# Performance work log

Measured on AMD Instinct MI355X. Metric: run time of the kernel, lower is better.

Reference implementation:

```python
import jax, jax.numpy as jnp
import numpy as np

NUM_HEADS = 16
HEAD_DIM = 64
INNER = NUM_HEADS * HEAD_DIM  # 1024
QUERY_DIM = 1024
CONTEXT_DIM = 768
SCALE = HEAD_DIM ** -0.5


def setup_inputs() -> dict:
    key = jax.random.key(0)
    ks = jax.random.split(key, 6)
    B, NQ, NKV = 8, 1024, 2048
    query = jax.random.normal(ks[0], (B, NQ, QUERY_DIM), dtype=jnp.float32)
    context = jax.random.normal(ks[1], (B, NKV, CONTEXT_DIM), dtype=jnp.float32)
    # weights stored as [in, out] (transpose of torch Linear), math-equivalent
    w_q = jax.random.normal(ks[2], (QUERY_DIM, INNER), dtype=jnp.float32) * (QUERY_DIM ** -0.5)
    w_kv = jax.random.normal(ks[3], (CONTEXT_DIM, 2 * INNER), dtype=jnp.float32) * (CONTEXT_DIM ** -0.5)
    w_out = jax.random.normal(ks[4], (INNER, QUERY_DIM), dtype=jnp.float32) * (INNER ** -0.5)
    b_out = jax.random.normal(ks[5], (QUERY_DIM,), dtype=jnp.float32) * 0.01
    return {"query": query, "context": context, "w_q": w_q, "w_kv": w_kv,
            "w_out": w_out, "b_out": b_out}


def reference(query, context, w_q, w_kv, w_out, b_out):
    B, NQ, _ = query.shape
    NKV = context.shape[1]
    q = query @ w_q                              # [B, NQ, INNER]
    kv = context @ w_kv                          # [B, NKV, 2*INNER]
    k, v = jnp.split(kv, 2, axis=-1)
    # reshape to [B, H, N, D]
    q = q.reshape(B, NQ, NUM_HEADS, HEAD_DIM).transpose(0, 2, 1, 3)
    k = k.reshape(B, NKV, NUM_HEADS, HEAD_DIM).transpose(0, 2, 1, 3)
    v = v.reshape(B, NKV, NUM_HEADS, HEAD_DIM).transpose(0, 2, 1, 3)
    scores = jnp.einsum('bhqd,bhkd->bhqk', q, k) * SCALE
    attn = jax.nn.softmax(scores, axis=-1)
    out = jnp.einsum('bhqk,bhkd->bhqd', attn, v)  # [B, H, NQ, D]
    out = out.transpose(0, 2, 1, 3).reshape(B, NQ, INNER)
    return out @ w_out + b_out
```

## Files before the change

kernel.cpp:

```cpp
#include <hip/hip_runtime.h>
#include <stdint.h>

typedef __bf16 bf16_t;
typedef bf16_t bf16x8 __attribute__((ext_vector_type(8)));
typedef float f32x4 __attribute__((ext_vector_type(4)));
typedef float f32x16 __attribute__((ext_vector_type(16)));
typedef unsigned uint32x2_t __attribute__((ext_vector_type(2)));
typedef unsigned uint32x4_t __attribute__((ext_vector_type(4)));

__device__ __forceinline__ unsigned short f2bf(float x) {
    unsigned u = __builtin_bit_cast(unsigned, x);
    u = (u + 0x7FFFu + ((u >> 16) & 1u)) >> 16;
    return (unsigned short)u;
}

__device__ __forceinline__ unsigned pk_bf16(float lo, float hi) {
    unsigned u0 = __builtin_bit_cast(unsigned, lo) + 0x8000u;
    unsigned u1 = __builtin_bit_cast(unsigned, hi) + 0x8000u;
    return __builtin_amdgcn_perm(u1, u0, 0x07060302u);
}

__device__ __forceinline__ void async_load16(const void* g, void* lds) {
    auto* gp = reinterpret_cast<const __attribute__((address_space(1))) uint32_t*>(
        reinterpret_cast<uintptr_t>(g));
    auto* lp = reinterpret_cast<__attribute__((address_space(3))) uint32_t*>(
        reinterpret_cast<uintptr_t>(lds));
    __builtin_amdgcn_global_load_lds(gp, lp, 16, 0, 0);
}

__global__ __launch_bounds__(256) void cast_f32_bf16(const float* __restrict__ src,
                                                     unsigned short* __restrict__ dst,
                                                     int n8) {
    int i = blockIdx.x * 256 + threadIdx.x;
    if (i >= n8) return;
    const float4* s4 = (const float4*)src;
    float4 a = s4[i * 2], b = s4[i * 2 + 1];
    uint4 o;
    o.x = (unsigned)f2bf(a.x) | ((unsigned)f2bf(a.y) << 16);
    o.y = (unsigned)f2bf(a.z) | ((unsigned)f2bf(a.w) << 16);
    o.z = (unsigned)f2bf(b.x) | ((unsigned)f2bf(b.y) << 16);
    o.w = (unsigned)f2bf(b.z) | ((unsigned)f2bf(b.w) << 16);
    ((uint4*)dst)[i] = o;
}

__global__ __launch_bounds__(256) void transcast(const float* __restrict__ src,
                                                 unsigned short* __restrict__ dst,
                                                 int K, int N, float scale) {
    __shared__ float tile[32][33];
    int x = threadIdx.x, y = threadIdx.y;
    int c0 = blockIdx.x * 32, r0 = blockIdx.y * 32;
    #pragma unroll
    for (int i = 0; i < 32; i += 8)
        tile[y + i][x] = src[(size_t)(r0 + y + i) * N + c0 + x];
    __syncthreads();
    #pragma unroll
    for (int i = 0; i < 32; i += 8)
        dst[(size_t)(c0 + y + i) * K + r0 + x] = f2bf(tile[x][y + i] * scale);
}

template <int EPI>
__global__ __launch_bounds__(256) void gemm_bt(const unsigned short* __restrict__ A,
                                               const unsigned short* __restrict__ Bt,
                                               void* __restrict__ Cout,
                                               const float* __restrict__ bias,
                                               int K, int N, int nkt) {
    __shared__ __align__(16) unsigned short lA[2][128 * 64];
    __shared__ __align__(16) unsigned short lB[2][128 * 64];
    const int tid = threadIdx.x;
    const int w = tid >> 6, l = tid & 63;
    const int wm = w >> 1, wn = w & 1;
    const int row0 = blockIdx.y * 128, col0 = blockIdx.x * 128;
    const int lrow = l & 15, lq = l >> 4;
    const int srow = l >> 3;
    const int scol = ((l & 7) ^ srow) * 8;

    f32x4 acc[4][4];
    #pragma unroll
    for (int i = 0; i < 4; ++i)
        #pragma unroll
        for (int j = 0; j < 4; ++j) acc[i][j] = (f32x4)0.f;

    const unsigned short* ga[4];
    const unsigned short* gb[4];
    #pragma unroll
    for (int q = 0; q < 4; ++q) {
        const int r = (w * 4 + q) * 8 + srow;
        ga[q] = A + (size_t)(row0 + r) * K + scol;
        gb[q] = Bt + (size_t)(col0 + r) * K + scol;
    }

    #pragma unroll
    for (int q = 0; q < 4; ++q) {
        async_load16(ga[q], (char*)lA + (w * 4 + q) * 1024);
        async_load16(gb[q], (char*)lB + (w * 4 + q) * 1024);
        ga[q] += 64;
        gb[q] += 64;
    }
    __syncthreads();

    for (int kt = 0; kt < nkt; ++kt) {
        const int bo = (kt & 1) * 16384;
        if (kt + 1 < nkt) {
            const int bn = bo ^ 16384;
            #pragma unroll
            for (int q = 0; q < 4; ++q) {
                async_load16(ga[q], (char*)lA + bn + (w * 4 + q) * 1024);
                async_load16(gb[q], (char*)lB + bn + (w * 4 + q) * 1024);
                ga[q] += 64;
                gb[q] += 64;
            }
        }
        #pragma unroll
        for (int kc = 0; kc < 2; ++kc) {
            const int pc = ((kc * 4 + lq) ^ (lrow & 7)) * 16;
            bf16x8 af[4], bfr[4];
            #pragma unroll
            for (int i = 0; i < 4; ++i)
                af[i] = *(const bf16x8*)((const char*)lA + bo + (wm * 64 + i * 16 + lrow) * 128 + pc);
            #pragma unroll
            for (int j = 0; j < 4; ++j)
                bfr[j] = *(const bf16x8*)((const char*)lB + bo + (wn * 64 + j * 16 + lrow) * 128 + pc);
            #pragma unroll
            for (int i = 0; i < 4; ++i)
                #pragma unroll
                for (int j = 0; j < 4; ++j)
                    acc[i][j] = __builtin_amdgcn_mfma_f32_16x16x32_bf16(af[i], bfr[j],
                                                                        acc[i][j], 0, 0, 0);
        }
        __syncthreads();
    }
    #pragma unroll
    for (int i = 0; i < 4; ++i) {
        const int grow0 = row0 + wm * 64 + i * 16 + lq * 4;
        #pragma unroll
        for (int j = 0; j < 4; ++j) {
            const int gcol = col0 + wn * 64 + j * 16 + lrow;
            #pragma unroll
            for (int r = 0; r < 4; ++r) {
                float v = acc[i][j][r];
                int grow = grow0 + r;
                if (EPI == 0) {
                    ((unsigned short*)Cout)[(size_t)grow * N + gcol] = f2bf(v);
                } else {
                    ((float*)Cout)[(size_t)grow * N + gcol] = v + bias[gcol];
                }
            }
        }
    }
}

__global__ __launch_bounds__(256, 2) void gemm_kv(const unsigned short* __restrict__ A,
                                                  const unsigned short* __restrict__ Bt,
                                                  unsigned short* __restrict__ Kb,
                                                  unsigned short* __restrict__ Vt) {
    __shared__ __align__(16) unsigned short lA[256 * 64];
    __shared__ __align__(16) unsigned short lB[128 * 64];
    const int tid = threadIdx.x;
    const int w = tid >> 6, l = tid & 63;
    const int wm = w >> 1, wn = w & 1;
    const int row0 = blockIdx.y * 256, col0 = blockIdx.x * 128;
    const int r32 = l & 31, hw = l >> 5;
    const int srow = l >> 3, scol = ((l & 7) ^ srow) * 8;

    f32x16 acc[4][2];
    #pragma unroll
    for (int mi = 0; mi < 4; ++mi)
        #pragma unroll
        for (int ni = 0; ni < 2; ++ni) acc[mi][ni] = (f32x16)0.f;

    const unsigned short* ga = A + (size_t)(row0 + w * 8 + srow) * 768 + scol;
    const unsigned short* gb = Bt + (size_t)(col0 + w * 8 + srow) * 768 + scol;
    char* lAw = (char*)lA + (w * 8) * 128;
    char* lBw = (char*)lB + (w * 8) * 128;
    const char* lap = (const char*)lA + (wm * 128 + r32) * 128;
    const char* lbp = (const char*)lB + (wn * 64 + r32) * 128;
    const int r7 = r32 & 7;

    for (int kt = 0; kt < 12; ++kt) {
        __syncthreads();
        #pragma unroll
        for (int q = 0; q < 8; ++q)
            async_load16(ga + (size_t)q * 32 * 768, lAw + q * 32 * 128);
        #pragma unroll
        for (int q = 0; q < 4; ++q)
            async_load16(gb + (size_t)q * 32 * 768, lBw + q * 32 * 128);
        ga += 64;
        gb += 64;
        __syncthreads();
        #pragma unroll
        for (int ks = 0; ks < 4; ++ks) {
            const int off = ((ks * 2 + hw) ^ r7) * 16;
            bf16x8 af[4], bfr[2];
            #pragma unroll
            for (int mi = 0; mi < 4; ++mi)
                af[mi] = *(const bf16x8*)(lap + mi * 32 * 128 + off);
            #pragma unroll
            for (int ni = 0; ni < 2; ++ni)
                bfr[ni] = *(const bf16x8*)(lbp + ni * 32 * 128 + off);
            #pragma unroll
            for (int mi = 0; mi < 4; ++mi)
                #pragma unroll
                for (int ni = 0; ni < 2; ++ni)
                    acc[mi][ni] = __builtin_amdgcn_mfma_f32_32x32x16_bf16(af[mi], bfr[ni],
                                                                          acc[mi][ni], 0, 0, 0);
        }
    }

    if (col0 < 1024) {
        unsigned short* kp = Kb + (size_t)(row0 + wm * 128) * 1024 + col0 + wn * 64 + r32;
        #pragma unroll
        for (int mi = 0; mi < 4; ++mi)
            #pragma unroll
            for (int ni = 0; ni < 2; ++ni)
                #pragma unroll
                for (int reg = 0; reg < 16; ++reg) {
                    int rr = mi * 32 + (reg & 3) + 8 * (reg >> 2) + 4 * hw;
                    kp[(size_t)rr * 1024 + ni * 32] = f2bf(acc[mi][ni][reg]);
                }
    } else {
        const int bb = row0 >> 11;
        const int keybase = (row0 & 2047) + wm * 128 + 4 * hw;
        const int fvbase = col0 - 1024 + wn * 64 + r32;
        unsigned short* vp = Vt + ((size_t)bb * 1024 + fvbase) * 2048 + keybase;
        #pragma unroll
        for (int mi = 0; mi < 4; ++mi)
            #pragma unroll
            for (int ni = 0; ni < 2; ++ni)
                #pragma unroll
                for (int g = 0; g < 4; ++g) {
                    uint2 pk2;
                    pk2.x = pk_bf16(acc[mi][ni][g * 4 + 0], acc[mi][ni][g * 4 + 1]);
                    pk2.y = pk_bf16(acc[mi][ni][g * 4 + 2], acc[mi][ni][g * 4 + 3]);
                    *(uint2*)(vp + (size_t)(ni * 32) * 2048 + mi * 32 + g * 8) = pk2;
                }
    }
}

__global__ __launch_bounds__(256, 4) void attn_fwd(const unsigned short* __restrict__ qb,
                                                   const unsigned short* __restrict__ kb,
                                                   const unsigned short* __restrict__ vt,
                                                   unsigned short* __restrict__ ob) {
    __shared__ __align__(16) unsigned short lK[2][64 * 64];
    __shared__ __align__(16) unsigned short lV[2][64 * 64];
    const int tid = threadIdx.x;
    const int w = tid >> 6, l = tid & 63;
    const int bh = blockIdx.x;
    const int b = bh >> 4, h = bh & 15;
    const int q0 = blockIdx.y * 128;
    const int lrow = l & 15, lq = l >> 4;
    const int srow = l >> 3, scol = ((l & 7) ^ (srow & 7)) * 8;

    bf16x8 bq[2][2];
    #pragma unroll
    for (int u = 0; u < 2; ++u)
        #pragma unroll
        for (int kc = 0; kc < 2; ++kc) {
            int row = b * 1024 + q0 + w * 32 + u * 16 + lrow;
            int col = h * 64 + kc * 32 + lq * 8;
            bq[u][kc] = *(const bf16x8*)(qb + (size_t)row * 1024 + col);
        }

    f32x4 ot[2][4];
    f32x4 lfr[2];
    #pragma unroll
    for (int u = 0; u < 2; ++u) {
        #pragma unroll
        for (int dt = 0; dt < 4; ++dt) ot[u][dt] = (f32x4)0.f;
        lfr[u] = (f32x4)0.f;
    }
    bf16x8 one8;
    #pragma unroll
    for (int i = 0; i < 8; ++i) one8[i] = (bf16_t)1.0f;

    const char* kp0 = (const char*)lK + lrow * 128 + ((lq ^ (lrow & 7)) * 16);
    const char* kp1 = (const char*)lK + lrow * 128 + (((4 + lq) ^ (lrow & 7)) * 16);
    const char* vp0 = (const char*)lV + lrow * 128 + ((lq ^ (lrow & 7)) * 16);
    const char* vp1 = (const char*)lV + lrow * 128 + (((4 + lq) ^ (lrow & 7)) * 16);

    const unsigned short* gkp = kb + (size_t)b * 2048 * 1024 + h * 64 +
                                (size_t)(w * 8 + srow) * 1024 + scol;
    const unsigned short* gvp = vt + (size_t)(b * 1024 + h * 64) * 2048 +
                                (size_t)(w * 8 + srow) * 2048 + scol;
    char* lKw0 = (char*)lK + (w * 8) * 128;
    char* lKw1 = (char*)lK + (32 + w * 8) * 128;
    char* lVw0 = (char*)lV + (w * 8) * 128;
    char* lVw1 = (char*)lV + (32 + w * 8) * 128;

    async_load16(gkp, lKw0);
    async_load16(gkp + 32 * 1024, lKw1);
    async_load16(gvp, lVw0);
    async_load16(gvp + 32 * 2048, lVw1);
    gkp += 64 * 1024;
    gvp += 64;
    __syncthreads();

    for (int it = 0; it < 32; ++it) {
        const int bo = (it & 1) * 8192;
        if (it < 31) {
            const int bn = bo ^ 8192;
            async_load16(gkp, lKw0 + bn);
            async_load16(gkp + 32 * 1024, lKw1 + bn);
            async_load16(gvp, lVw0 + bn);
            async_load16(gvp + 32 * 2048, lVw1 + bn);
            gkp += 64 * 1024;
            gvp += 64;
        }

        bf16x8 ka[4][2];
        #pragma unroll
        for (int mt = 0; mt < 4; ++mt) {
            ka[mt][0] = *(const bf16x8*)(kp0 + bo + mt * 2048);
            ka[mt][1] = *(const bf16x8*)(kp1 + bo + mt * 2048);
        }

        unsigned D[2][4][2];
        __builtin_amdgcn_s_setprio(1);
        #pragma unroll
        for (int u = 0; u < 2; ++u) {
            #pragma unroll
            for (int mt = 0; mt < 4; ++mt) {
                f32x4 c = (f32x4)0.f;
                c = __builtin_amdgcn_mfma_f32_16x16x32_bf16(ka[mt][0], bq[u][0], c, 0, 0, 0);
                c = __builtin_amdgcn_mfma_f32_16x16x32_bf16(ka[mt][1], bq[u][1], c, 0, 0, 0);
                #pragma unroll
                for (int r = 0; r < 4; ++r)
                    c[r] = __builtin_amdgcn_exp2f(c[r]);
                D[u][mt][0] = pk_bf16(c[0], c[1]);
                D[u][mt][1] = pk_bf16(c[2], c[3]);
            }
        }
        __builtin_amdgcn_s_setprio(0);

        bf16x8 pb[2][2];
        #pragma unroll
        for (int u = 0; u < 2; ++u) {
            uint32x4_t pbw[2];
            #pragma unroll
            for (int half = 0; half < 2; ++half) {
                #pragma unroll
                for (int r2 = 0; r2 < 2; ++r2) {
                    uint32x2_t t = __builtin_amdgcn_permlane32_swap(
                        D[u][half * 2][r2], D[u][half * 2 + 1][r2], false, false);
                    uint32x2_t z = __builtin_amdgcn_permlane16_swap(t.x, t.y, false, false);
                    pbw[half][r2] = z.x;
                    pbw[half][r2 + 2] = z.y;
                }
            }
            pb[u][0] = __builtin_bit_cast(bf16x8, pbw[0]);
            pb[u][1] = __builtin_bit_cast(bf16x8, pbw[1]);
        }

        bf16x8 va[4][2];
        #pragma unroll
        for (int dt = 0; dt < 4; ++dt) {
            va[dt][0] = *(const bf16x8*)(vp0 + bo + dt * 2048);
            va[dt][1] = *(const bf16x8*)(vp1 + bo + dt * 2048);
        }

        __builtin_amdgcn_s_setprio(1);
        #pragma unroll
        for (int u = 0; u < 2; ++u) {
            lfr[u] = __builtin_amdgcn_mfma_f32_16x16x32_bf16(one8, pb[u][0], lfr[u], 0, 0, 0);
            lfr[u] = __builtin_amdgcn_mfma_f32_16x16x32_bf16(one8, pb[u][1], lfr[u], 0, 0, 0);
            #pragma unroll
            for (int dt = 0; dt < 4; ++dt) {
                ot[u][dt] = __builtin_amdgcn_mfma_f32_16x16x32_bf16(va[dt][0], pb[u][0], ot[u][dt], 0, 0, 0);
                ot[u][dt] = __builtin_amdgcn_mfma_f32_16x16x32_bf16(va[dt][1], pb[u][1], ot[u][dt], 0, 0, 0);
            }
        }
        __builtin_amdgcn_s_setprio(0);
        __syncthreads();
    }

    #pragma unroll
    for (int u = 0; u < 2; ++u) {
        float inv = 1.f / lfr[u][0];
        size_t grow = (size_t)(b * 1024 + q0 + w * 32 + u * 16 + lrow);
        unsigned short* op = ob + grow * 1024 + h * 64 + 4 * lq;
        #pragma unroll
        for (int dt = 0; dt < 4; ++dt) {
            uint2 pk;
            pk.x = pk_bf16(ot[u][dt][0] * inv, ot[u][dt][1] * inv);
            pk.y = pk_bf16(ot[u][dt][2] * inv, ot[u][dt][3] * inv);
            *(uint2*)(op + 16 * dt) = pk;
        }
    }
}

extern "C" void kernel_launch(void* const* d_in, const int* in_sizes, int n_in,
                              void* d_out, int out_size, void* d_ws, size_t ws_size,
                              hipStream_t stream) {
    const float* query   = (const float*)d_in[0];
    const float* context = (const float*)d_in[1];
    const float* w_q     = (const float*)d_in[2];
    const float* w_kv    = (const float*)d_in[3];
    const float* w_out   = (const float*)d_in[4];
    const float* b_out   = (const float*)d_in[5];
    float* out = (float*)d_out;

    char* p = (char*)d_ws;
    unsigned short* qin   = (unsigned short*)p; p += (size_t)8192 * 1024 * 2;
    unsigned short* cin   = (unsigned short*)p; p += (size_t)16384 * 768 * 2;
    unsigned short* wqT   = (unsigned short*)p; p += (size_t)1024 * 1024 * 2;
    unsigned short* wkvT  = (unsigned short*)p; p += (size_t)2048 * 768 * 2;
    unsigned short* woutT = (unsigned short*)p; p += (size_t)1024 * 1024 * 2;
    unsigned short* qproj = (unsigned short*)p; p += (size_t)8192 * 1024 * 2;
    unsigned short* kbuf  = (unsigned short*)p; p += (size_t)16384 * 1024 * 2;
    unsigned short* vT    = (unsigned short*)p; p += (size_t)16384 * 1024 * 2;
    unsigned short* obuf  = (unsigned short*)p; p += (size_t)8192 * 1024 * 2;

    const float qscale = 0.125f * 1.44269504088896f;

    cast_f32_bf16<<<8388608 / 8 / 256, 256, 0, stream>>>(query, qin, 8388608 / 8);
    cast_f32_bf16<<<12582912 / 8 / 256, 256, 0, stream>>>(context, cin, 12582912 / 8);
    transcast<<<dim3(32, 32), dim3(32, 8), 0, stream>>>(w_q, wqT, 1024, 1024, qscale);
    transcast<<<dim3(64, 24), dim3(32, 8), 0, stream>>>(w_kv, wkvT, 768, 2048, 1.0f);
    transcast<<<dim3(32, 32), dim3(32, 8), 0, stream>>>(w_out, woutT, 1024, 1024, 1.0f);
    gemm_bt<0><<<dim3(8, 64), 256, 0, stream>>>(qin, wqT, qproj, nullptr, 1024, 1024, 16);
    gemm_kv<<<dim3(16, 64), 256, 0, stream>>>(cin, wkvT, kbuf, vT);
    attn_fwd<<<dim3(128, 8), 256, 0, stream>>>(qproj, kbuf, vT, obuf);
    gemm_bt<2><<<dim3(8, 64), 256, 0, stream>>>(obuf, woutT, out, b_out, 1024, 1024, 16);
}
```

Baseline: 332.4 us.

## Fuse prep kernels, double-buffer smaller KV GEMM tiles, halve attention query tile

Merges the two casts and three weight transposes into one launch that dispatches on block index, which cuts launch overhead. The KV projection GEMM moves from 256x128 single-buffered tiles to 128x128 double-buffered tiles, prefetching the next K slice during MFMA work and doubling the grid. Attention blocks now cover 64 query rows instead of 128, with each wave holding one 16-row fragment. This doubles the grid and raises the occupancy target to 5, at the cost of loading each K/V tile twice as often per query row.

```diff
diff --git a/kernel.cpp b/kernel.cpp
--- a/kernel.cpp
+++ b/kernel.cpp
@@ -28,11 +28,8 @@
     __builtin_amdgcn_global_load_lds(gp, lp, 16, 0, 0);
 }
 
-__global__ __launch_bounds__(256) void cast_f32_bf16(const float* __restrict__ src,
-                                                     unsigned short* __restrict__ dst,
-                                                     int n8) {
-    int i = blockIdx.x * 256 + threadIdx.x;
-    if (i >= n8) return;
+__device__ __forceinline__ void cast8(const float* __restrict__ src,
+                                      unsigned short* __restrict__ dst, int i) {
     const float4* s4 = (const float4*)src;
     float4 a = s4[i * 2], b = s4[i * 2 + 1];
     uint4 o;
@@ -43,12 +40,12 @@
     ((uint4*)dst)[i] = o;
 }
 
-__global__ __launch_bounds__(256) void transcast(const float* __restrict__ src,
-                                                 unsigned short* __restrict__ dst,
-                                                 int K, int N, float scale) {
-    __shared__ float tile[32][33];
-    int x = threadIdx.x, y = threadIdx.y;
-    int c0 = blockIdx.x * 32, r0 = blockIdx.y * 32;
+__device__ __forceinline__ void transcast_body(const float* __restrict__ src,
+                                               unsigned short* __restrict__ dst,
+                                               int K, int N, float scale,
+                                               int bx, int by, float (*tile)[33],
+                                               int x, int y) {
+    int c0 = bx * 32, r0 = by * 32;
     #pragma unroll
     for (int i = 0; i < 32; i += 8)
         tile[y + i][x] = src[(size_t)(r0 + y + i) * N + c0 + x];
@@ -56,6 +53,36 @@
     #pragma unroll
     for (int i = 0; i < 32; i += 8)
         dst[(size_t)(c0 + y + i) * K + r0 + x] = f2bf(tile[x][y + i] * scale);
+}
+
+__global__ __launch_bounds__(256) void prep(const float* __restrict__ query,
+                                            const float* __restrict__ context,
+                                            const float* __restrict__ w_q,
+                                            const float* __restrict__ w_kv,
+                                            const float* __restrict__ w_out,
+                                            unsigned short* __restrict__ qin,
+                                            unsigned short* __restrict__ cin,
+                                            unsigned short* __restrict__ wqT,
+                                            unsigned short* __restrict__ wkvT,
+                                            unsigned short* __restrict__ woutT,
+                                            float qscale) {
+    __shared__ float tile[32][33];
+    const int blk = blockIdx.x, tid = threadIdx.x;
+    const int x = tid & 31, y = tid >> 5;
+    if (blk < 4096) {
+        cast8(query, qin, blk * 256 + tid);
+    } else if (blk < 10240) {
+        cast8(context, cin, (blk - 4096) * 256 + tid);
+    } else if (blk < 11264) {
+        int lb = blk - 10240;
+        transcast_body(w_q, wqT, 1024, 1024, qscale, lb & 31, lb >> 5, tile, x, y);
+    } else if (blk < 12800) {
+        int lb = blk - 11264;
+        transcast_body(w_kv, wkvT, 768, 2048, 1.0f, lb & 63, lb >> 6, tile, x, y);
+    } else {
+        int lb = blk - 12800;
+        transcast_body(w_out, woutT, 1024, 1024, 1.0f, lb & 31, lb >> 5, tile, x, y);
+    }
 }
 
 template <int EPI>
@@ -153,63 +180,72 @@
                                                   const unsigned short* __restrict__ Bt,
                                                   unsigned short* __restrict__ Kb,
                                                   unsigned short* __restrict__ Vt) {
-    __shared__ __align__(16) unsigned short lA[256 * 64];
-    __shared__ __align__(16) unsigned short lB[128 * 64];
+    __shared__ __align__(16) unsigned short lA[2][128 * 64];
+    __shared__ __align__(16) unsigned short lB[2][128 * 64];
     const int tid = threadIdx.x;
     const int w = tid >> 6, l = tid & 63;
     const int wm = w >> 1, wn = w & 1;
-    const int row0 = blockIdx.y * 256, col0 = blockIdx.x * 128;
+    const int row0 = blockIdx.y * 128, col0 = blockIdx.x * 128;
     const int r32 = l & 31, hw = l >> 5;
     const int srow = l >> 3, scol = ((l & 7) ^ srow) * 8;
-
-    f32x16 acc[4][2];
-    #pragma unroll
-    for (int mi = 0; mi < 4; ++mi)
+    const int r7 = r32 & 7;
+
+    f32x16 acc[2][2];
+    #pragma unroll
+    for (int mi = 0; mi < 2; ++mi)
         #pragma unroll
         for (int ni = 0; ni < 2; ++ni) acc[mi][ni] = (f32x16)0.f;
 
     const unsigned short* ga = A + (size_t)(row0 + w * 8 + srow) * 768 + scol;
     const unsigned short* gb = Bt + (size_t)(col0 + w * 8 + srow) * 768 + scol;
-    char* lAw = (char*)lA + (w * 8) * 128;
-    char* lBw = (char*)lB + (w * 8) * 128;
-    const char* lap = (const char*)lA + (wm * 128 + r32) * 128;
+    const char* lap = (const char*)lA + (wm * 64 + r32) * 128;
     const char* lbp = (const char*)lB + (wn * 64 + r32) * 128;
-    const int r7 = r32 & 7;
+
+    #pragma unroll
+    for (int q = 0; q < 4; ++q) {
+        async_load16(ga + (size_t)q * 32 * 768, (char*)lA + (q * 32 + w * 8) * 128);
+        async_load16(gb + (size_t)q * 32 * 768, (char*)lB + (q * 32 + w * 8) * 128);
+    }
+    ga += 64;
+    gb += 64;
+    __syncthreads();
 
     for (int kt = 0; kt < 12; ++kt) {
-        __syncthreads();
-        #pragma unroll
-        for (int q = 0; q < 8; ++q)
-            async_load16(ga + (size_t)q * 32 * 768, lAw + q * 32 * 128);
-        #pragma unroll
-        for (int q = 0; q < 4; ++q)
-            async_load16(gb + (size_t)q * 32 * 768, lBw + q * 32 * 128);
-        ga += 64;
-        gb += 64;
-        __syncthreads();
+        const int bo = (kt & 1) * 16384;
+        if (kt < 11) {
+            const int bn = bo ^ 16384;
+            #pragma unroll
+            for (int q = 0; q < 4; ++q) {
+                async_load16(ga + (size_t)q * 32 * 768, (char*)lA + bn + (q * 32 + w * 8) * 128);
+                async_load16(gb + (size_t)q * 32 * 768, (char*)lB + bn + (q * 32 + w * 8) * 128);
+            }
+            ga += 64;
+            gb += 64;
+        }
         #pragma unroll
         for (int ks = 0; ks < 4; ++ks) {
             const int off = ((ks * 2 + hw) ^ r7) * 16;
-            bf16x8 af[4], bfr[2];
-            #pragma unroll
-            for (int mi = 0; mi < 4; ++mi)
-                af[mi] = *(const bf16x8*)(lap + mi * 32 * 128 + off);
+            bf16x8 af[2], bfr[2];
+            #pragma unroll
+            for (int mi = 0; mi < 2; ++mi)
+                af[mi] = *(const bf16x8*)(lap + bo + mi * 32 * 128 + off);
             #pragma unroll
             for (int ni = 0; ni < 2; ++ni)
-                bfr[ni] = *(const bf16x8*)(lbp + ni * 32 * 128 + off);
-            #pragma unroll
-            for (int mi = 0; mi < 4; ++mi)
+                bfr[ni] = *(const bf16x8*)(lbp + bo + ni * 32 * 128 + off);
+            #pragma unroll
+            for (int mi = 0; mi < 2; ++mi)
                 #pragma unroll
                 for (int ni = 0; ni < 2; ++ni)
                     acc[mi][ni] = __builtin_amdgcn_mfma_f32_32x32x16_bf16(af[mi], bfr[ni],
                                                                           acc[mi][ni], 0, 0, 0);
         }
+        __syncthreads();
     }
 
     if (col0 < 1024) {
-        unsigned short* kp = Kb + (size_t)(row0 + wm * 128) * 1024 + col0 + wn * 64 + r32;
-        #pragma unroll
-        for (int mi = 0; mi < 4; ++mi)
+        unsigned short* kp = Kb + (size_t)(row0 + wm * 64) * 1024 + col0 + wn * 64 + r32;
+        #pragma unroll
+        for (int mi = 0; mi < 2; ++mi)
             #pragma unroll
             for (int ni = 0; ni < 2; ++ni)
                 #pragma unroll
@@ -219,11 +255,11 @@
                 }
     } else {
         const int bb = row0 >> 11;
-        const int keybase = (row0 & 2047) + wm * 128 + 4 * hw;
+        const int keybase = (row0 & 2047) + wm * 64 + 4 * hw;
         const int fvbase = col0 - 1024 + wn * 64 + r32;
         unsigned short* vp = Vt + ((size_t)bb * 1024 + fvbase) * 2048 + keybase;
         #pragma unroll
-        for (int mi = 0; mi < 4; ++mi)
+        for (int mi = 0; mi < 2; ++mi)
             #pragma unroll
             for (int ni = 0; ni < 2; ++ni)
                 #pragma unroll
@@ -236,7 +272,7 @@
     }
 }
 
-__global__ __launch_bounds__(256, 4) void attn_fwd(const unsigned short* __restrict__ qb,
+__global__ __launch_bounds__(256, 5) void attn_fwd(const unsigned short* __restrict__ qb,
                                                    const unsigned short* __restrict__ kb,
                                                    const unsigned short* __restrict__ vt,
                                                    unsigned short* __restrict__ ob) {
@@ -246,28 +282,22 @@
     const int w = tid >> 6, l = tid & 63;
     const int bh = blockIdx.x;
     const int b = bh >> 4, h = bh & 15;
-    const int q0 = blockIdx.y * 128;
+    const int q0 = blockIdx.y * 64;
     const int lrow = l & 15, lq = l >> 4;
     const int srow = l >> 3, scol = ((l & 7) ^ (srow & 7)) * 8;
 
-    bf16x8 bq[2][2];
-    #pragma unroll
-    for (int u = 0; u < 2; ++u)
-        #pragma unroll
-        for (int kc = 0; kc < 2; ++kc) {
-            int row = b * 1024 + q0 + w * 32 + u * 16 + lrow;
-            int col = h * 64 + kc * 32 + lq * 8;
-            bq[u][kc] = *(const bf16x8*)(qb + (size_t)row * 1024 + col);
-        }
-
-    f32x4 ot[2][4];
-    f32x4 lfr[2];
-    #pragma unroll
-    for (int u = 0; u < 2; ++u) {
-        #pragma unroll
-        for (int dt = 0; dt < 4; ++dt) ot[u][dt] = (f32x4)0.f;
-        lfr[u] = (f32x4)0.f;
-    }
+    bf16x8 bq[2];
+    #pragma unroll
+    for (int kc = 0; kc < 2; ++kc) {
+        int row = b * 1024 + q0 + w * 16 + lrow;
+        int col = h * 64 + kc * 32 + lq * 8;
+        bq[kc] = *(const bf16x8*)(qb + (size_t)row * 1024 + col);
+    }
+
+    f32x4 ot[4];
+    f32x4 lfr = (f32x4)0.f;
+    #pragma unroll
+    for (int dt = 0; dt < 4; ++dt) ot[dt] = (f32x4)0.f;
     bf16x8 one8;
     #pragma unroll
     for (int i = 0; i < 8; ++i) one8[i] = (bf16_t)1.0f;
@@ -313,41 +343,37 @@
             ka[mt][1] = *(const bf16x8*)(kp1 + bo + mt * 2048);
         }
 
-        unsigned D[2][4][2];
+        unsigned D[4][2];
         __builtin_amdgcn_s_setprio(1);
         #pragma unroll
-        for (int u = 0; u < 2; ++u) {
-            #pragma unroll
-            for (int mt = 0; mt < 4; ++mt) {
-                f32x4 c = (f32x4)0.f;
-                c = __builtin_amdgcn_mfma_f32_16x16x32_bf16(ka[mt][0], bq[u][0], c, 0, 0, 0);
-                c = __builtin_amdgcn_mfma_f32_16x16x32_bf16(ka[mt][1], bq[u][1], c, 0, 0, 0);
-                #pragma unroll
-                for (int r = 0; r < 4; ++r)
-                    c[r] = __builtin_amdgcn_exp2f(c[r]);
-                D[u][mt][0] = pk_bf16(c[0], c[1]);
-                D[u][mt][1] = pk_bf16(c[2], c[3]);
-            }
+        for (int mt = 0; mt < 4; ++mt) {
+            f32x4 c = (f32x4)0.f;
+            c = __builtin_amdgcn_mfma_f32_16x16x32_bf16(ka[mt][0], bq[0], c, 0, 0, 0);
+            c = __builtin_amdgcn_mfma_f32_16x16x32_bf16(ka[mt][1], bq[1], c, 0, 0, 0);
+            #pragma unroll
+            for (int r = 0; r < 4; ++r)
+                c[r] = __builtin_amdgcn_exp2f(c[r]);
+            D[mt][0] = pk_bf16(c[0], c[1]);
+            D[mt][1] = pk_bf16(c[2], c[3]);
         }
         __builtin_amdgcn_s_setprio(0);
 
-        bf16x8 pb[2][2];
-        #pragma unroll
-        for (int u = 0; u < 2; ++u) {
+        bf16x8 pb[2];
+        {
             uint32x4_t pbw[2];
             #pragma unroll
             for (int half = 0; half < 2; ++half) {
                 #pragma unroll
                 for (int r2 = 0; r2 < 2; ++r2) {
                     uint32x2_t t = __builtin_amdgcn_permlane32_swap(
-                        D[u][half * 2][r2], D[u][half * 2 + 1][r2], false, false);
+                        D[half * 2][r2], D[half * 2 + 1][r2], false, false);
                     uint32x2_t z = __builtin_amdgcn_permlane16_swap(t.x, t.y, false, false);
                     pbw[half][r2] = z.x;
                     pbw[half][r2 + 2] = z.y;
                 }
             }
-            pb[u][0] = __builtin_bit_cast(bf16x8, pbw[0]);
-            pb[u][1] = __builtin_bit_cast(bf16x8, pbw[1]);
+            pb[0] = __builtin_bit_cast(bf16x8, pbw[0]);
+            pb[1] = __builtin_bit_cast(bf16x8, pbw[1]);
         }
 
         bf16x8 va[4][2];
@@ -358,30 +384,26 @@
         }
 
         __builtin_amdgcn_s_setprio(1);
-        #pragma unroll
-        for (int u = 0; u < 2; ++u) {
-            lfr[u] = __builtin_amdgcn_mfma_f32_16x16x32_bf16(one8, pb[u][0], lfr[u], 0, 0, 0);
-            lfr[u] = __builtin_amdgcn_mfma_f32_16x16x32_bf16(one8, pb[u][1], lfr[u], 0, 0, 0);
-            #pragma unroll
-            for (int dt = 0; dt < 4; ++dt) {
-                ot[u][dt] = __builtin_amdgcn_mfma_f32_16x16x32_bf16(va[dt][0], pb[u][0], ot[u][dt], 0, 0, 0);
-                ot[u][dt] = __builtin_amdgcn_mfma_f32_16x16x32_bf16(va[dt][1], pb[u][1], ot[u][dt], 0, 0, 0);
-            }
+        lfr = __builtin_amdgcn_mfma_f32_16x16x32_bf16(one8, pb[0], lfr, 0, 0, 0);
+        lfr = __builtin_amdgcn_mfma_f32_16x16x32_bf16(one8, pb[1], lfr, 0, 0, 0);
+        #pragma unroll
+        for (int dt = 0; dt < 4; ++dt) {
+            ot[dt] = __builtin_amdgcn_mfma_f32_16x16x32_bf16(va[dt][0], pb[0], ot[dt], 0, 0, 0);
+            ot[dt] = __builtin_amdgcn_mfma_f32_16x16x32_bf16(va[dt][1], pb[1], ot[dt], 0, 0, 0);
         }
         __builtin_amdgcn_s_setprio(0);
         __syncthreads();
     }
 
-    #pragma unroll
-    for (int u = 0; u < 2; ++u) {
-        float inv = 1.f / lfr[u][0];
-        size_t grow = (size_t)(b * 1024 + q0 + w * 32 + u * 16 + lrow);
+    {
+        float inv = 1.f / lfr[0];
+        size_t grow = (size_t)(b * 1024 + q0 + w * 16 + lrow);
         unsigned short* op = ob + grow * 1024 + h * 64 + 4 * lq;
         #pragma unroll
         for (int dt = 0; dt < 4; ++dt) {
             uint2 pk;
-            pk.x = pk_bf16(ot[u][dt][0] * inv, ot[u][dt][1] * inv);
-            pk.y = pk_bf16(ot[u][dt][2] * inv, ot[u][dt][3] * inv);
+            pk.x = pk_bf16(ot[dt][0] * inv, ot[dt][1] * inv);
+            pk.y = pk_bf16(ot[dt][2] * inv, ot[dt][3] * inv);
             *(uint2*)(op + 16 * dt) = pk;
         }
     }
@@ -411,13 +433,10 @@
 
     const float qscale = 0.125f * 1.44269504088896f;
 
-    cast_f32_bf16<<<8388608 / 8 / 256, 256, 0, stream>>>(query, qin, 8388608 / 8);
-    cast_f32_bf16<<<12582912 / 8 / 256, 256, 0, stream>>>(context, cin, 12582912 / 8);
-    transcast<<<dim3(32, 32), dim3(32, 8), 0, stream>>>(w_q, wqT, 1024, 1024, qscale);
-    transcast<<<dim3(64, 24), dim3(32, 8), 0, stream>>>(w_kv, wkvT, 768, 2048, 1.0f);
-    transcast<<<dim3(32, 32), dim3(32, 8), 0, stream>>>(w_out, woutT, 1024, 1024, 1.0f);
+    prep<<<13824, 256, 0, stream>>>(query, context, w_q, w_kv, w_out,
+                                    qin, cin, wqT, wkvT, woutT, qscale);
     gemm_bt<0><<<dim3(8, 64), 256, 0, stream>>>(qin, wqT, qproj, nullptr, 1024, 1024, 16);
-    gemm_kv<<<dim3(16, 64), 256, 0, stream>>>(cin, wkvT, kbuf, vT);
-    attn_fwd<<<dim3(128, 8), 256, 0, stream>>>(qproj, kbuf, vT, obuf);
+    gemm_kv<<<dim3(16, 128), 256, 0, stream>>>(cin, wkvT, kbuf, vT);
+    attn_fwd<<<dim3(128, 16), 256, 0, stream>>>(qproj, kbuf, vT, obuf);
     gemm_bt<2><<<dim3(8, 64), 256, 0, stream>>>(obuf, woutT, out, b_out, 1024, 1024, 16);
 }
```

New measurement: 333.3 us. About the same (+0.3%).

## Fuse prep kernels and retile GEMMs with 512-thread double-buffered pipelines

Applied to the files above, without the earlier changes.

Merges the two casts and three weight transposes into one prep launch to cut launch overhead. The Q/out GEMMs move to 256x128 tiles with 8 waves and 32x32 MFMAs. The KV GEMM moves to 256x256 tiles with 8 waves. Both GEMMs now use a two-stage async LDS pipeline with explicit vmcnt waits in place of load-then-sync. This adds LDS use per block and leaves one block per CU, and it depends on the hand-written waitcnt counts being correct.

```diff
diff --git a/kernel.cpp b/kernel.cpp
--- a/kernel.cpp
+++ b/kernel.cpp
@@ -28,11 +28,8 @@
     __builtin_amdgcn_global_load_lds(gp, lp, 16, 0, 0);
 }
 
-__global__ __launch_bounds__(256) void cast_f32_bf16(const float* __restrict__ src,
-                                                     unsigned short* __restrict__ dst,
-                                                     int n8) {
-    int i = blockIdx.x * 256 + threadIdx.x;
-    if (i >= n8) return;
+__device__ __forceinline__ void cast8(const float* __restrict__ src,
+                                      unsigned short* __restrict__ dst, int i) {
     const float4* s4 = (const float4*)src;
     float4 a = s4[i * 2], b = s4[i * 2 + 1];
     uint4 o;
@@ -43,12 +40,12 @@
     ((uint4*)dst)[i] = o;
 }
 
-__global__ __launch_bounds__(256) void transcast(const float* __restrict__ src,
-                                                 unsigned short* __restrict__ dst,
-                                                 int K, int N, float scale) {
-    __shared__ float tile[32][33];
-    int x = threadIdx.x, y = threadIdx.y;
-    int c0 = blockIdx.x * 32, r0 = blockIdx.y * 32;
+__device__ __forceinline__ void transcast_body(const float* __restrict__ src,
+                                               unsigned short* __restrict__ dst,
+                                               int K, int N, float scale,
+                                               int bx, int by, float (*tile)[33],
+                                               int x, int y) {
+    int c0 = bx * 32, r0 = by * 32;
     #pragma unroll
     for (int i = 0; i < 32; i += 8)
         tile[y + i][x] = src[(size_t)(r0 + y + i) * N + c0 + x];
@@ -58,109 +55,144 @@
         dst[(size_t)(c0 + y + i) * K + r0 + x] = f2bf(tile[x][y + i] * scale);
 }
 
+__global__ __launch_bounds__(256) void prep(const float* __restrict__ query,
+                                            const float* __restrict__ context,
+                                            const float* __restrict__ w_q,
+                                            const float* __restrict__ w_kv,
+                                            const float* __restrict__ w_out,
+                                            unsigned short* __restrict__ qin,
+                                            unsigned short* __restrict__ cin,
+                                            unsigned short* __restrict__ wqT,
+                                            unsigned short* __restrict__ wkvT,
+                                            unsigned short* __restrict__ woutT,
+                                            float qscale) {
+    __shared__ float tile[32][33];
+    const int blk = blockIdx.x, tid = threadIdx.x;
+    const int x = tid & 31, y = tid >> 5;
+    if (blk < 4096) {
+        cast8(query, qin, blk * 256 + tid);
+    } else if (blk < 10240) {
+        cast8(context, cin, (blk - 4096) * 256 + tid);
+    } else if (blk < 11264) {
+        int lb = blk - 10240;
+        transcast_body(w_q, wqT, 1024, 1024, qscale, lb & 31, lb >> 5, tile, x, y);
+    } else if (blk < 12800) {
+        int lb = blk - 11264;
+        transcast_body(w_kv, wkvT, 768, 2048, 1.0f, lb & 63, lb >> 6, tile, x, y);
+    } else {
+        int lb = blk - 12800;
+        transcast_body(w_out, woutT, 1024, 1024, 1.0f, lb & 31, lb >> 5, tile, x, y);
+    }
+}
+
 template <int EPI>
-__global__ __launch_bounds__(256) void gemm_bt(const unsigned short* __restrict__ A,
-                                               const unsigned short* __restrict__ Bt,
-                                               void* __restrict__ Cout,
-                                               const float* __restrict__ bias,
-                                               int K, int N, int nkt) {
-    __shared__ __align__(16) unsigned short lA[2][128 * 64];
+__global__ __launch_bounds__(512, 1) void gemm_bt(const unsigned short* __restrict__ A,
+                                                  const unsigned short* __restrict__ Bt,
+                                                  void* __restrict__ Cout,
+                                                  const float* __restrict__ bias) {
+    __shared__ __align__(16) unsigned short lA[2][256 * 64];
     __shared__ __align__(16) unsigned short lB[2][128 * 64];
-    const int tid = threadIdx.x;
-    const int w = tid >> 6, l = tid & 63;
-    const int wm = w >> 1, wn = w & 1;
-    const int row0 = blockIdx.y * 128, col0 = blockIdx.x * 128;
-    const int lrow = l & 15, lq = l >> 4;
-    const int srow = l >> 3;
-    const int scol = ((l & 7) ^ srow) * 8;
-
-    f32x4 acc[4][4];
-    #pragma unroll
-    for (int i = 0; i < 4; ++i)
-        #pragma unroll
-        for (int j = 0; j < 4; ++j) acc[i][j] = (f32x4)0.f;
-
-    const unsigned short* ga[4];
-    const unsigned short* gb[4];
-    #pragma unroll
-    for (int q = 0; q < 4; ++q) {
-        const int r = (w * 4 + q) * 8 + srow;
-        ga[q] = A + (size_t)(row0 + r) * K + scol;
-        gb[q] = Bt + (size_t)(col0 + r) * K + scol;
-    }
-
-    #pragma unroll
-    for (int q = 0; q < 4; ++q) {
-        async_load16(ga[q], (char*)lA + (w * 4 + q) * 1024);
-        async_load16(gb[q], (char*)lB + (w * 4 + q) * 1024);
-        ga[q] += 64;
-        gb[q] += 64;
-    }
-    __syncthreads();
-
-    for (int kt = 0; kt < nkt; ++kt) {
-        const int bo = (kt & 1) * 16384;
-        if (kt + 1 < nkt) {
-            const int bn = bo ^ 16384;
-            #pragma unroll
-            for (int q = 0; q < 4; ++q) {
-                async_load16(ga[q], (char*)lA + bn + (w * 4 + q) * 1024);
-                async_load16(gb[q], (char*)lB + bn + (w * 4 + q) * 1024);
-                ga[q] += 64;
-                gb[q] += 64;
-            }
-        }
-        #pragma unroll
-        for (int kc = 0; kc < 2; ++kc) {
-            const int pc = ((kc * 4 + lq) ^ (lrow & 7)) * 16;
-            bf16x8 af[4], bfr[4];
-            #pragma unroll
-            for (int i = 0; i < 4; ++i)
-                af[i] = *(const bf16x8*)((const char*)lA + bo + (wm * 64 + i * 16 + lrow) * 128 + pc);
-            #pragma unroll
-            for (int j = 0; j < 4; ++j)
-                bfr[j] = *(const bf16x8*)((const char*)lB + bo + (wn * 64 + j * 16 + lrow) * 128 + pc);
-            #pragma unroll
-            for (int i = 0; i < 4; ++i)
-                #pragma unroll
-                for (int j = 0; j < 4; ++j)
-                    acc[i][j] = __builtin_amdgcn_mfma_f32_16x16x32_bf16(af[i], bfr[j],
-                                                                        acc[i][j], 0, 0, 0);
-        }
-        __syncthreads();
-    }
-    #pragma unroll
-    for (int i = 0; i < 4; ++i) {
-        const int grow0 = row0 + wm * 64 + i * 16 + lq * 4;
-        #pragma unroll
-        for (int j = 0; j < 4; ++j) {
-            const int gcol = col0 + wn * 64 + j * 16 + lrow;
-            #pragma unroll
-            for (int r = 0; r < 4; ++r) {
-                float v = acc[i][j][r];
-                int grow = grow0 + r;
-                if (EPI == 0) {
-                    ((unsigned short*)Cout)[(size_t)grow * N + gcol] = f2bf(v);
-                } else {
-                    ((float*)Cout)[(size_t)grow * N + gcol] = v + bias[gcol];
-                }
-            }
-        }
-    }
-}
-
-__global__ __launch_bounds__(256, 2) void gemm_kv(const unsigned short* __restrict__ A,
-                                                  const unsigned short* __restrict__ Bt,
-                                                  unsigned short* __restrict__ Kb,
-                                                  unsigned short* __restrict__ Vt) {
-    __shared__ __align__(16) unsigned short lA[256 * 64];
-    __shared__ __align__(16) unsigned short lB[128 * 64];
     const int tid = threadIdx.x;
     const int w = tid >> 6, l = tid & 63;
     const int wm = w >> 1, wn = w & 1;
     const int row0 = blockIdx.y * 256, col0 = blockIdx.x * 128;
     const int r32 = l & 31, hw = l >> 5;
     const int srow = l >> 3, scol = ((l & 7) ^ srow) * 8;
+    const int r7 = r32 & 7;
+
+    f32x16 acc[2][2];
+    #pragma unroll
+    for (int mi = 0; mi < 2; ++mi)
+        #pragma unroll
+        for (int ni = 0; ni < 2; ++ni) acc[mi][ni] = (f32x16)0.f;
+
+    const unsigned short* ga = A + (size_t)(row0 + w * 8 + srow) * 1024 + scol;
+    const unsigned short* gb = Bt + (size_t)(col0 + w * 8 + srow) * 1024 + scol;
+    const char* lap = (const char*)lA + (wm * 64 + r32) * 128;
+    const char* lbp = (const char*)lB + (wn * 64 + r32) * 128;
+
+    auto stage = [&](int kt, int buf) {
+        const unsigned short* a = ga + kt * 64;
+        const unsigned short* bsrc = gb + kt * 64;
+        char* la = (char*)lA + buf * 32768 + (w * 8) * 128;
+        char* lb = (char*)lB + buf * 16384 + (w * 8) * 128;
+        #pragma unroll
+        for (int q = 0; q < 4; ++q)
+            async_load16(a + (size_t)q * 64 * 1024, la + q * 64 * 128);
+        #pragma unroll
+        for (int q = 0; q < 2; ++q)
+            async_load16(bsrc + (size_t)q * 64 * 1024, lb + q * 64 * 128);
+    };
+    auto compute = [&](int buf) {
+        const char* ap = lap + buf * 32768;
+        const char* bp = lbp + buf * 16384;
+        #pragma unroll
+        for (int ks = 0; ks < 4; ++ks) {
+            const int off = ((ks * 2 + hw) ^ r7) * 16;
+            bf16x8 af[2], bfr[2];
+            #pragma unroll
+            for (int mi = 0; mi < 2; ++mi)
+                af[mi] = *(const bf16x8*)(ap + mi * 32 * 128 + off);
+            #pragma unroll
+            for (int ni = 0; ni < 2; ++ni)
+                bfr[ni] = *(const bf16x8*)(bp + ni * 32 * 128 + off);
+            #pragma unroll
+            for (int mi = 0; mi < 2; ++mi)
+                #pragma unroll
+                for (int ni = 0; ni < 2; ++ni)
+                    acc[mi][ni] = __builtin_amdgcn_mfma_f32_32x32x16_bf16(af[mi], bfr[ni],
+                                                                          acc[mi][ni], 0, 0, 0);
+        }
+    };
+
+    stage(0, 0);
+    stage(1, 1);
+    #pragma unroll 1
+    for (int kt = 0; kt < 14; ++kt) {
+        asm volatile("s_waitcnt vmcnt(6)" ::: "memory");
+        __builtin_amdgcn_s_barrier();
+        compute(kt & 1);
+        asm volatile("" ::: "memory");
+        __builtin_amdgcn_s_barrier();
+        stage(kt + 2, kt & 1);
+    }
+    asm volatile("s_waitcnt vmcnt(6)" ::: "memory");
+    __builtin_amdgcn_s_barrier();
+    compute(0);
+    asm volatile("s_waitcnt vmcnt(0)" ::: "memory");
+    __builtin_amdgcn_s_barrier();
+    compute(1);
+
+    #pragma unroll
+    for (int mi = 0; mi < 2; ++mi)
+        #pragma unroll
+        for (int ni = 0; ni < 2; ++ni)
+            #pragma unroll
+            for (int reg = 0; reg < 16; ++reg) {
+                const int row = row0 + wm * 64 + mi * 32 + (reg & 3) + 8 * (reg >> 2) + 4 * hw;
+                const int col = col0 + wn * 64 + ni * 32 + r32;
+                float v = acc[mi][ni][reg];
+                if (EPI == 0) {
+                    ((unsigned short*)Cout)[(size_t)row * 1024 + col] = f2bf(v);
+                } else {
+                    ((float*)Cout)[(size_t)row * 1024 + col] = v + bias[col];
+                }
+            }
+}
+
+__global__ __launch_bounds__(512, 1) void gemm_kv(const unsigned short* __restrict__ A,
+                                                  const unsigned short* __restrict__ Bt,
+                                                  unsigned short* __restrict__ Kb,
+                                                  unsigned short* __restrict__ Vt) {
+    __shared__ __align__(16) unsigned short lA[2][256 * 64];
+    __shared__ __align__(16) unsigned short lB[2][256 * 64];
+    const int tid = threadIdx.x;
+    const int w = tid >> 6, l = tid & 63;
+    const int wm = w >> 2, wn = w & 3;
+    const int row0 = blockIdx.y * 256, col0 = blockIdx.x * 256;
+    const int r32 = l & 31, hw = l >> 5;
+    const int srow = l >> 3, scol = ((l & 7) ^ srow) * 8;
+    const int r7 = r32 & 7;
 
     f32x16 acc[4][2];
     #pragma unroll
@@ -170,33 +202,33 @@
 
     const unsigned short* ga = A + (size_t)(row0 + w * 8 + srow) * 768 + scol;
     const unsigned short* gb = Bt + (size_t)(col0 + w * 8 + srow) * 768 + scol;
-    char* lAw = (char*)lA + (w * 8) * 128;
-    char* lBw = (char*)lB + (w * 8) * 128;
     const char* lap = (const char*)lA + (wm * 128 + r32) * 128;
     const char* lbp = (const char*)lB + (wn * 64 + r32) * 128;
-    const int r7 = r32 & 7;
-
-    for (int kt = 0; kt < 12; ++kt) {
-        __syncthreads();
-        #pragma unroll
-        for (int q = 0; q < 8; ++q)
-            async_load16(ga + (size_t)q * 32 * 768, lAw + q * 32 * 128);
-        #pragma unroll
-        for (int q = 0; q < 4; ++q)
-            async_load16(gb + (size_t)q * 32 * 768, lBw + q * 32 * 128);
-        ga += 64;
-        gb += 64;
-        __syncthreads();
+
+    auto stage = [&](int kt, int buf) {
+        const unsigned short* a = ga + kt * 64;
+        const unsigned short* bsrc = gb + kt * 64;
+        char* la = (char*)lA + buf * 32768 + (w * 8) * 128;
+        char* lb = (char*)lB + buf * 32768 + (w * 8) * 128;
+        #pragma unroll
+        for (int q = 0; q < 4; ++q) {
+            async_load16(a + (size_t)q * 64 * 768, la + q * 64 * 128);
+            async_load16(bsrc + (size_t)q * 64 * 768, lb + q * 64 * 128);
+        }
+    };
+    auto compute = [&](int buf) {
+        const char* ap = lap + buf * 32768;
+        const char* bp = lbp + buf * 32768;
         #pragma unroll
         for (int ks = 0; ks < 4; ++ks) {
             const int off = ((ks * 2 + hw) ^ r7) * 16;
             bf16x8 af[4], bfr[2];
             #pragma unroll
             for (int mi = 0; mi < 4; ++mi)
-                af[mi] = *(const bf16x8*)(lap + mi * 32 * 128 + off);
+                af[mi] = *(const bf16x8*)(ap + mi * 32 * 128 + off);
             #pragma unroll
             for (int ni = 0; ni < 2; ++ni)
-                bfr[ni] = *(const bf16x8*)(lbp + ni * 32 * 128 + off);
+                bfr[ni] = *(const bf16x8*)(bp + ni * 32 * 128 + off);
             #pragma unroll
             for (int mi = 0; mi < 4; ++mi)
                 #pragma unroll
@@ -204,7 +236,25 @@
                     acc[mi][ni] = __builtin_amdgcn_mfma_f32_32x32x16_bf16(af[mi], bfr[ni],
                                                                           acc[mi][ni], 0, 0, 0);
         }
-    }
+    };
+
+    stage(0, 0);
+    stage(1, 1);
+    #pragma unroll 1
+    for (int kt = 0; kt < 10; ++kt) {
+        asm volatile("s_waitcnt vmcnt(8)" ::: "memory");
+        __builtin_amdgcn_s_barrier();
+        compute(kt & 1);
+        asm volatile("" ::: "memory");
+        __builtin_amdgcn_s_barrier();
+        stage(kt + 2, kt & 1);
+    }
+    asm volatile("s_waitcnt vmcnt(8)" ::: "memory");
+    __builtin_amdgcn_s_barrier();
+    compute(0);
+    asm volatile("s_waitcnt vmcnt(0)" ::: "memory");
+    __builtin_amdgcn_s_barrier();
+    compute(1);
 
     if (col0 < 1024) {
         unsigned short* kp = Kb + (size_t)(row0 + wm * 128) * 1024 + col0 + wn * 64 + r32;
@@ -411,13 +461,10 @@
 
     const float qscale = 0.125f * 1.44269504088896f;
 
-    cast_f32_bf16<<<8388608 / 8 / 256, 256, 0, stream>>>(query, qin, 8388608 / 8);
-    cast_f32_bf16<<<12582912 / 8 / 256, 256, 0, stream>>>(context, cin, 12582912 / 8);
-    transcast<<<dim3(32, 32), dim3(32, 8), 0, stream>>>(w_q, wqT, 1024, 1024, qscale);
-    transcast<<<dim3(64, 24), dim3(32, 8), 0, stream>>>(w_kv, wkvT, 768, 2048, 1.0f);
-    transcast<<<dim3(32, 32), dim3(32, 8), 0, stream>>>(w_out, woutT, 1024, 1024, 1.0f);
-    gemm_bt<0><<<dim3(8, 64), 256, 0, stream>>>(qin, wqT, qproj, nullptr, 1024, 1024, 16);
-    gemm_kv<<<dim3(16, 64), 256, 0, stream>>>(cin, wkvT, kbuf, vT);
+    prep<<<13824, 256, 0, stream>>>(query, context, w_q, w_kv, w_out,
+                                    qin, cin, wqT, wkvT, woutT, qscale);
+    gemm_bt<0><<<dim3(8, 32), 512, 0, stream>>>(qin, wqT, qproj, nullptr);
+    gemm_kv<<<dim3(8, 64), 512, 0, stream>>>(cin, wkvT, kbuf, vT);
     attn_fwd<<<dim3(128, 8), 256, 0, stream>>>(qproj, kbuf, vT, obuf);
-    gemm_bt<2><<<dim3(8, 64), 256, 0, stream>>>(obuf, woutT, out, b_out, 1024, 1024, 16);
-}
+    gemm_bt<2><<<dim3(8, 32), 512, 0, stream>>>(obuf, woutT, out, b_out);
+}
```

Result: no change. 334.4 us (+0.6%).
